# Kernel optimization log

Measured on AMD Instinct MI355X. Metric: run time of the kernel, lower is better.

Reference implementation:

```python
import jax, jax.numpy as jnp
import numpy as np

B, NQ, NK = 4, 2048, 2048
D_MODEL, D_K, D_V, H = 1024, 1024, 1024, 16


def setup_inputs() -> dict:
    key = jax.random.key(0)
    ks = jax.random.split(key, 8)
    return {
        "queries": jax.random.normal(ks[0], (B, NQ, D_MODEL), dtype=jnp.float32),
        "keys": jax.random.normal(ks[1], (B, NK, D_MODEL), dtype=jnp.float32),
        "values": jax.random.normal(ks[2], (B, NK, D_MODEL), dtype=jnp.float32),
        # nn.Linear weights init.normal_(std=0.001); stored here in (in, out) layout
        "Wq": jax.random.normal(ks[3], (D_MODEL, D_K), dtype=jnp.float32) * 0.001,
        "Wk": jax.random.normal(ks[4], (D_MODEL, D_K), dtype=jnp.float32) * 0.001,
        "Wv": jax.random.normal(ks[5], (D_MODEL, D_V), dtype=jnp.float32) * 0.001,
        "Wo": jax.random.normal(ks[6], (D_V, D_MODEL), dtype=jnp.float32) * 0.001,
        "bo": jnp.zeros((D_MODEL,), dtype=jnp.float32),
    }


def reference(queries, keys, values, Wq, Wk, Wv, Wo, bo):
    b_s, nq, _ = queries.shape
    nk = keys.shape[1]
    hd_k = D_K // H  # per-head key dim
    hd_v = D_V // H  # per-head value dim
    # projections -> [b, h, n, hd]
    q = (queries @ Wq).reshape(b_s, nq, H, hd_k).transpose(0, 2, 1, 3)
    k = (keys @ Wk).reshape(b_s, nk, H, hd_k).transpose(0, 2, 1, 3)
    v = (values @ Wv).reshape(b_s, nk, H, hd_v).transpose(0, 2, 1, 3)
    # NOTE: original scales by sqrt(d_k) (full d_k), not per-head dim
    att = jnp.einsum("bhqd,bhkd->bhqk", q, k) / np.float32(np.sqrt(D_K))
    att = jax.nn.softmax(att, axis=-1)
    # dropout = identity (eval mode)
    out = jnp.einsum("bhqk,bhkd->bhqd", att, v)
    out = out.transpose(0, 2, 1, 3).reshape(b_s, nq, D_V)
    return out @ Wo + bo
```

## Files before the change

kernel.cpp:

```cpp
#include <hip/hip_runtime.h>


#define DM    1024
#define NSEQ  2048
#define HEADS 16
#define HD    64

typedef float floatx4 __attribute__((ext_vector_type(4)));
typedef short s16x4   __attribute__((ext_vector_type(4)));
typedef short s16x8   __attribute__((ext_vector_type(8)));
typedef unsigned int u32x4 __attribute__((ext_vector_type(4)));

static __device__ __forceinline__ floatx4 mfma_bf16(s16x8 a, s16x8 b, floatx4 c) {
  return __builtin_amdgcn_mfma_f32_16x16x32_bf16(a, b, c, 0, 0, 0);
}

static __device__ __forceinline__ void gload_lds16(const void* g, void* l) {
  __builtin_amdgcn_global_load_lds(
      (const __attribute__((address_space(1))) unsigned*)g,
      (__attribute__((address_space(3))) unsigned*)l, 16, 0, 0);
}

static __device__ __forceinline__ unsigned lds_addr(const void* p) {
  return (unsigned)(unsigned long long)p;
}

static __device__ __forceinline__ s16x8 ds_read_b128a(unsigned byteaddr) {
  s16x8 r;
  asm volatile("ds_read_b128 %0, %1" : "=v"(r) : "v"(byteaddr));
  return r;
}

#define SCHED0() __builtin_amdgcn_sched_barrier(0)
#define WAIT_LGKM0() \
  { asm volatile("s_waitcnt lgkmcnt(0)" ::: "memory"); __builtin_amdgcn_sched_barrier(0); }
#define WAIT_VMCNT(N) \
  { asm volatile("s_waitcnt vmcnt(" #N ")" ::: "memory"); __builtin_amdgcn_sched_barrier(0); }

static __device__ __forceinline__ short f2bf(float f) {
  unsigned u = __builtin_bit_cast(unsigned, f);
  u += 0x7FFFu + ((u >> 16) & 1u);
  return (short)(u >> 16);
}

static __device__ __forceinline__ unsigned cvtpk_bf16(float lo, float hi) {
  unsigned r;
  asm("v_cvt_pk_bf16_f32 %0, %1, %2" : "=v"(r) : "v"(lo), "v"(hi));
  return r;
}

static __device__ __forceinline__ unsigned pack2_bf16(float a, float b) {
  unsigned ua = __builtin_bit_cast(unsigned, a) + 0x8000u;
  unsigned ub = __builtin_bit_cast(unsigned, b) + 0x8000u;
#if __has_builtin(__builtin_amdgcn_perm)
  return __builtin_amdgcn_perm(ub, ua, 0x07060302u);
#else
  return (ub & 0xffff0000u) | (ua >> 16);
#endif
}

__global__ __launch_bounds__(256) void make_wgroups(
    const float* __restrict__ W0, const float* __restrict__ W1,
    const float* __restrict__ W2, const float* __restrict__ W3,
    short* __restrict__ G0, short* __restrict__ G1,
    short* __restrict__ G2, short* __restrict__ G3) {
  __shared__ float tile[64][68];
  const int m = blockIdx.z;
  const float* W = m == 0 ? W0 : m == 1 ? W1 : m == 2 ? W2 : W3;
  short*       G = m == 0 ? G0 : m == 1 ? G1 : m == 2 ? G2 : G3;
  const int nt = blockIdx.x, kt = blockIdx.y;
  const int n0 = nt * 64, k0 = kt * 64;
  const int t = threadIdx.x;
  for (int j = 0; j < 4; j++) {
    int idx = j * 256 + t, r = idx >> 4, cq = idx & 15;
    *(floatx4*)&tile[r][cq * 4] = *(const floatx4*)(W + (long)(k0 + r) * DM + n0 + cq * 4);
  }
  __syncthreads();
  for (int j = 0; j < 2; j++) {
    int ci = j * 256 + t;
    int lm = ci & 15, quad = (ci >> 4) & 3, kk = (ci >> 6) & 1, gl = ci >> 7;
    s16x8 v;
#pragma unroll
    for (int e = 0; e < 8; e++) v[e] = f2bf(tile[kk * 32 + quad * 8 + e][gl * 16 + lm]);
    long addr;
    if (m < 3) {
      int ct = nt >> 2, g16 = (nt & 3) * 4 + gl;
      addr = ((long)(ct * 16 + kt)) * 16384 + (g16 * 2 + kk) * 512 + (quad * 16 + lm) * 8;
    } else {
      int ct = nt >> 1, g16 = (nt & 1) * 4 + gl;
      addr = ((long)(ct * 16 + kt)) * 8192 + (g16 * 2 + kk) * 512 + (quad * 16 + lm) * 8;
    }
    *(s16x8*)(G + addr) = v;
  }
}

__global__ __launch_bounds__(512, 2) void proj_kernel(
    const float* __restrict__ Aq, const float* __restrict__ Ak, const float* __restrict__ Av,
    const short* __restrict__ BgQ, const short* __restrict__ BgK, const short* __restrict__ BgV,
    short* __restrict__ Qh, short* __restrict__ KVg) {
  __shared__ short lds[2 * 24576];
  const int z = blockIdx.z;
  const float* A  = z == 0 ? Aq  : z == 1 ? Ak  : Av;
  const short* Bg = z == 0 ? BgQ : z == 1 ? BgK : BgV;
  const int t = threadIdx.x;
  const int w = t >> 6, l = t & 63, quad = l >> 4, lm = l & 15;
  const int wm = w >> 2, wn = w & 3;
  const int row0 = blockIdx.x * 128;
  const int ct = blockIdx.y;
  const int col0 = ct * 256;

  floatx4 acc[4][4];
  for (int mi = 0; mi < 4; mi++)
    for (int ni = 0; ni < 4; ni++) acc[mi][ni] = (floatx4){0.f, 0.f, 0.f, 0.f};

  floatx4 ar[2][2];
  auto loadA = [&](int ks) __attribute__((always_inline)) {
#pragma unroll
    for (int j = 0; j < 2; j++) {
      int tt = j * 512 + t, r = tt >> 3, c8 = (tt & 7) * 8;
      const float* p = A + (long)(row0 + r) * DM + ks * 64 + c8;
      ar[j][0] = *(const floatx4*)p;
      ar[j][1] = *(const floatx4*)(p + 4);
    }
  };
  auto writeA = [&](int buf) __attribute__((always_inline)) {
#pragma unroll
    for (int j = 0; j < 2; j++) {
      int tt = j * 512 + t, r = tt >> 3;
      int kk = (tt & 7) >> 2, q4 = tt & 3, lm2 = r & 15, g16 = r >> 4;
      u32x4 pk = {cvtpk_bf16(ar[j][0][0], ar[j][0][1]), cvtpk_bf16(ar[j][0][2], ar[j][0][3]),
                  cvtpk_bf16(ar[j][1][0], ar[j][1][1]), cvtpk_bf16(ar[j][1][2], ar[j][1][3])};
      int l3 = q4 * 16 + (lm2 ^ (q4 * 2));
      *(s16x8*)(lds + buf * 24576 + (g16 * 2 + kk) * 512 + l3 * 8) =
          __builtin_bit_cast(s16x8, pk);
    }
  };
  auto stageB = [&](int ks, int buf) __attribute__((always_inline)) {
    const long pan = ((long)(ct * 16 + ks)) * 16384;
#pragma unroll
    for (int i = 0; i < 4; i++) {
      int gb = w * 4 + i;
      const short* src = Bg + pan + gb * 512 + l * 8;
      gload_lds16(src, lds + buf * 24576 + 8192 + gb * 512);
    }
  };

  const unsigned lds0 = lds_addr(lds);
  auto process = [&](int buf) __attribute__((always_inline)) {
    const unsigned lbase = lds0 + buf * 49152u;
    const unsigned aswz = (quad * 16 + (lm ^ (quad * 2))) * 16;
#pragma unroll
    for (int kk = 0; kk < 2; kk++) {
      s16x8 af[4], bfr[4];
#pragma unroll
      for (int mi = 0; mi < 4; mi++)
        af[mi] = ds_read_b128a(lbase + ((wm * 4 + mi) * 2 + kk) * 1024 + aswz);
#pragma unroll
      for (int ni = 0; ni < 4; ni++)
        bfr[ni] = ds_read_b128a(lbase + 16384 + ((wn * 4 + ni) * 2 + kk) * 1024 + l * 16);
      WAIT_LGKM0();
      __builtin_amdgcn_s_setprio(1);
#pragma unroll
      for (int mi = 0; mi < 4; mi++)
#pragma unroll
        for (int ni = 0; ni < 4; ni++)
          acc[mi][ni] = mfma_bf16(af[mi], bfr[ni], acc[mi][ni]);
      __builtin_amdgcn_s_setprio(0);
    }
  };

  loadA(0);
  stageB(0, 0);
  writeA(0);
  __syncthreads();
  int cur = 0;
  for (int ks = 0; ks < 16; ++ks) {
    if (ks + 1 < 16) { loadA(ks + 1); stageB(ks + 1, cur ^ 1); }
    SCHED0();
    process(cur);
    if (ks + 1 < 16) writeA(cur ^ 1);
    __syncthreads();
    cur ^= 1;
  }

  const int rowbase = row0 + wm * 64;
  const int colbase = col0 + wn * 64;
  const int b = rowbase >> 11;
  const int h = colbase >> 6;
  const int rloc = rowbase & 2047;
  if (z == 0) {
    const float osc = 0.0450842200277801f;
    long base = ((long)(b * HEADS + h)) * NSEQ * HD;
    for (int mi = 0; mi < 4; mi++)
      for (int r = 0; r < 4; r++) {
        int q = rloc + mi * 16 + quad * 4 + r;
        long rowoff = base + (long)q * HD + lm;
        for (int ni = 0; ni < 4; ni++)
          Qh[rowoff + ni * 16] = f2bf(acc[mi][ni][r] * osc);
      }
  } else if (z == 1) {
    long bhb = ((long)(b * HEADS + h)) * 262144;
    for (int mi = 0; mi < 4; mi++)
      for (int r = 0; r < 4; r++) {
        int q = rloc + mi * 16 + quad * 4 + r;
        int tile = q >> 7, s = (q >> 5) & 3, jj = (q >> 4) & 1, lmk = q & 15;
        for (int ni = 0; ni < 4; ni++) {
          int c = ni >> 1, quadk = (ni * 2 + (lm >> 3)) & 3, ek = lm & 7;
          long addr = bhb + (long)tile * 16384 + (s * 4 + jj * 2 + c) * 512 +
                      (quadk * 16 + lmk) * 8 + ek;
          KVg[addr] = f2bf(acc[mi][ni][r]);
        }
      }
  } else {
    long bhb = ((long)(b * HEADS + h)) * 262144;
    for (int mi = 0; mi < 4; mi++)
      for (int r = 0; r < 4; r++) {
        int kc = rloc + (mi >> 1) * 32 + quad * 8 + (mi & 1) * 4 + r;
        int tile = kc >> 7, s = (kc >> 5) & 3, ev = (mi & 1) * 4 + r;
        for (int ni = 0; ni < 4; ni++) {
          long addr = bhb + (long)tile * 16384 + (16 + s * 4 + ni) * 512 +
                      (quad * 16 + lm) * 8 + ev;
          KVg[addr] = f2bf(acc[mi][ni][r]);
        }
      }
  }
}

__global__ __launch_bounds__(512, 2) void attn_kernel(
    const short* __restrict__ Qh, const short* __restrict__ KVg,
    short* __restrict__ Obf) {
  __shared__ short lds[2 * 16384];
  const int t = threadIdx.x;
  const int w = t >> 6, l = t & 63, quad = l >> 4, lm = l & 15;
  const int bh = blockIdx.x;
  const int qtile = blockIdx.y * 256 + w * 32;
  const short* Qp  = Qh  + (long)bh * NSEQ * HD;
  const short* KVp = KVg + (long)bh * 262144;

  s16x8 aq[2][2];
#pragma unroll
  for (int qi = 0; qi < 2; qi++)
#pragma unroll
    for (int c = 0; c < 2; c++)
      aq[qi][c] = *(const s16x8*)(Qp + (long)(qtile + qi * 16 + lm) * HD + c * 32 + quad * 8);

  floatx4 acc[2][4];
  float lsum[2] = {0.f, 0.f};
#pragma unroll
  for (int qi = 0; qi < 2; qi++)
#pragma unroll
    for (int n = 0; n < 4; n++) acc[qi][n] = (floatx4){0.f, 0.f, 0.f, 0.f};

  auto stage = [&](int kt, int buf) __attribute__((always_inline)) {
    short* base = lds + buf * 16384;
    const short* tsrc = KVp + (long)(kt >> 7) * 16384;
#pragma unroll
    for (int i = 0; i < 4; i++) {
      int g = w * 4 + i;
      gload_lds16(tsrc + g * 512 + l * 8, base + g * 512);
    }
  };

  auto process = [&](const short* Lb, int s) __attribute__((always_inline)) {
    s16x8 bk[2][2];
#pragma unroll
    for (int j = 0; j < 2; j++)
#pragma unroll
      for (int c = 0; c < 2; c++)
        bk[j][c] = *(const s16x8*)(Lb + ((s * 4 + j * 2 + c) * 64 + l) * 8);
    s16x8 vraw[4];
#pragma unroll
    for (int n = 0; n < 4; n++)
      vraw[n] = *(const s16x8*)(Lb + ((16 + s * 4 + n) * 64 + l) * 8);
#pragma unroll
    for (int qi = 0; qi < 2; qi++) {
      floatx4 sT[2];
      sT[0] = (floatx4){0.f, 0.f, 0.f, 0.f};
      sT[1] = (floatx4){0.f, 0.f, 0.f, 0.f};
      __builtin_amdgcn_s_setprio(1);
#pragma unroll
      for (int c = 0; c < 2; c++) {
        sT[0] = mfma_bf16(bk[0][c], aq[qi][c], sT[0]);
        sT[1] = mfma_bf16(bk[1][c], aq[qi][c], sT[1]);
      }
      __builtin_amdgcn_s_setprio(0);
      float p0 = __builtin_amdgcn_exp2f(sT[0][0]);
      float p1 = __builtin_amdgcn_exp2f(sT[0][1]);
      float p2 = __builtin_amdgcn_exp2f(sT[0][2]);
      float p3 = __builtin_amdgcn_exp2f(sT[0][3]);
      float p4 = __builtin_amdgcn_exp2f(sT[1][0]);
      float p5 = __builtin_amdgcn_exp2f(sT[1][1]);
      float p6 = __builtin_amdgcn_exp2f(sT[1][2]);
      float p7 = __builtin_amdgcn_exp2f(sT[1][3]);
      lsum[qi] += ((p0 + p1) + (p2 + p3)) + ((p4 + p5) + (p6 + p7));
      u32x4 pw = {pack2_bf16(p0, p1), pack2_bf16(p2, p3),
                  pack2_bf16(p4, p5), pack2_bf16(p6, p7)};
      s16x8 pcat = __builtin_bit_cast(s16x8, pw);
      __builtin_amdgcn_s_setprio(1);
#pragma unroll
      for (int n = 0; n < 4; n++)
        acc[qi][n] = mfma_bf16(vraw[n], pcat, acc[qi][n]);
      __builtin_amdgcn_s_setprio(0);
    }
  };

  stage(0, 0);
  __syncthreads();
  int cur = 0;
  for (int kt = 0; kt < NSEQ; kt += 128) {
    if (kt + 128 < NSEQ) stage(kt + 128, cur ^ 1);
    const short* Lb = lds + cur * 16384;
    process(Lb, 0);
    process(Lb, 1);
    process(Lb, 2);
    process(Lb, 3);
    __syncthreads();
    cur ^= 1;
  }

  const int b = bh >> 4, h = bh & 15;
  short* Ow = lds + w * 1152;
  const int erow = l >> 2, ecg = l & 3;
#pragma unroll
  for (int qi = 0; qi < 2; qi++) {
    float ls = lsum[qi];
    ls += __shfl_xor(ls, 16);
    ls += __shfl_xor(ls, 32);
    float rl = 1.0f / ls;
#pragma unroll
    for (int n = 0; n < 4; n++)
#pragma unroll
      for (int r = 0; r < 4; r++)
        Ow[lm * 72 + n * 16 + quad * 4 + r] = f2bf(acc[qi][n][r] * rl);
    s16x8 o0 = *(const s16x8*)(Ow + erow * 72 + ecg * 16);
    s16x8 o1 = *(const s16x8*)(Ow + erow * 72 + ecg * 16 + 8);
    long gaddr = ((long)(b * NSEQ + qtile + qi * 16 + erow)) * DM + h * HD + ecg * 16;
    *(s16x8*)(Obf + gaddr) = o0;
    *(s16x8*)(Obf + gaddr + 8) = o1;
  }
}

__global__ __launch_bounds__(256, 2) void out_kernel(
    const short* __restrict__ Ab, const short* __restrict__ WoG,
    const float* __restrict__ bias, float* __restrict__ Out) {
  __shared__ short lds[3 * 8192];
  const int t = threadIdx.x;
  const int w = t >> 6, l = t & 63, quad = l >> 4, lm = l & 15;
  const int wm = w >> 1, wn = w & 1;
  const int row0 = blockIdx.x * 128;
  const int ct = blockIdx.y;
  const int col0 = ct * 128;

  floatx4 acc[4][4];
  for (int mi = 0; mi < 4; mi++)
    for (int ni = 0; ni < 4; ni++) acc[mi][ni] = (floatx4){0.f, 0.f, 0.f, 0.f};

  s16x8 ar[2];
  auto loadA = [&](int kt) __attribute__((always_inline)) {
#pragma unroll
    for (int j = 0; j < 2; j++) {
      int tt = j * 256 + t, r = tt >> 2, c = tt & 3;
      ar[j] = *(const s16x8*)(Ab + (long)(row0 + r) * DM + kt * 32 + c * 8);
    }
  };
  auto writeA = [&](int buf) __attribute__((always_inline)) {
#pragma unroll
    for (int j = 0; j < 2; j++) {
      int tt = j * 256 + t, r = tt >> 2, q4 = tt & 3;
      int lm2 = r & 15, g16 = r >> 4;
      int l3 = q4 * 16 + (lm2 ^ (q4 * 2));
      *(s16x8*)(lds + buf * 8192 + g16 * 512 + l3 * 8) = ar[j];
    }
  };
  auto stageB = [&](int kt, int buf) __attribute__((always_inline)) {
    const long pan = ((long)(ct * 16 + (kt >> 1))) * 8192;
    const int kk = kt & 1;
#pragma unroll
    for (int i = 0; i < 2; i++) {
      int gb = w * 2 + i;
      const short* src = WoG + pan + (gb * 2 + kk) * 512 + l * 8;
      gload_lds16(src, lds + buf * 8192 + 4096 + gb * 512);
    }
  };
  const unsigned lds0 = lds_addr(lds);
  auto process = [&](int buf) __attribute__((always_inline)) {
    const unsigned lbase = lds0 + buf * 16384;
    const unsigned aswz = (quad * 16 + (lm ^ (quad * 2))) * 16;
    s16x8 af[4], bfr[4];
#pragma unroll
    for (int mi = 0; mi < 4; mi++)
      af[mi] = ds_read_b128a(lbase + (wm * 4 + mi) * 1024 + aswz);
#pragma unroll
    for (int ni = 0; ni < 4; ni++)
      bfr[ni] = ds_read_b128a(lbase + 8192 + (wn * 4 + ni) * 1024 + l * 16);
    WAIT_LGKM0();
    __builtin_amdgcn_s_setprio(1);
#pragma unroll
    for (int mi = 0; mi < 4; mi++)
#pragma unroll
      for (int ni = 0; ni < 4; ni++)
        acc[mi][ni] = mfma_bf16(af[mi], bfr[ni], acc[mi][ni]);
    __builtin_amdgcn_s_setprio(0);
  };

  loadA(0);
  stageB(0, 0);
  stageB(1, 1);
  writeA(0);
  WAIT_VMCNT(2);
  WAIT_LGKM0();
  __builtin_amdgcn_s_barrier();

  for (int kt = 0; kt < 32; ++kt) {
    if (kt + 1 < 32) loadA(kt + 1);
    if (kt + 2 < 32) stageB(kt + 2, (kt + 2) % 3);
    SCHED0();
    process(kt % 3);
    if (kt + 1 < 32) writeA((kt + 1) % 3);
    WAIT_VMCNT(2);
    WAIT_LGKM0();
    __builtin_amdgcn_s_barrier();
  }

  const int rowbase = row0 + wm * 64;
  const int colbase = col0 + wn * 64;
  for (int mi = 0; mi < 4; mi++)
    for (int r = 0; r < 4; r++) {
      int gr = rowbase + mi * 16 + quad * 4 + r;
      for (int ni = 0; ni < 4; ni++) {
        int gc = colbase + ni * 16 + lm;
        Out[(long)gr * DM + gc] = acc[mi][ni][r] + bias[gc];
      }
    }
}

extern "C" void kernel_launch(void* const* d_in, const int* in_sizes, int n_in,
                              void* d_out, int out_size, void* d_ws, size_t ws_size,
                              hipStream_t stream) {
  (void)in_sizes; (void)n_in; (void)out_size; (void)ws_size;
  const float* queries = (const float*)d_in[0];
  const float* keys    = (const float*)d_in[1];
  const float* values  = (const float*)d_in[2];
  const float* Wq = (const float*)d_in[3];
  const float* Wk = (const float*)d_in[4];
  const float* Wv = (const float*)d_in[5];
  const float* Wo = (const float*)d_in[6];
  const float* bo = (const float*)d_in[7];
  float* out = (float*)d_out;

  char* ws = (char*)d_ws;
  const size_t MB = 1024 * 1024;
  short* WqG = (short*)(ws + 0 * MB);
  short* WkG = (short*)(ws + 2 * MB);
  short* WvG = (short*)(ws + 4 * MB);
  short* WoG = (short*)(ws + 6 * MB);
  short* Qh  = (short*)(ws + 8 * MB);
  short* KVg = (short*)(ws + 24 * MB);
  short* Obf = (short*)(ws + 56 * MB);

  make_wgroups<<<dim3(16, 16, 4), 256, 0, stream>>>(
      Wq, Wk, Wv, Wo, WqG, WkG, WvG, WoG);
  proj_kernel<<<dim3(64, 4, 3), 512, 0, stream>>>(
      queries, keys, values, WqG, WkG, WvG, Qh, KVg);
  attn_kernel<<<dim3(64, 8), 512, 0, stream>>>(Qh, KVg, Obf);
  out_kernel<<<dim3(64, 8), 256, 0, stream>>>(Obf, WoG, bo, out);
}
```

Measured before the change: 318.9 us.

## Read K/V tiles directly from global memory instead of LDS double buffering

Removes the LDS staging of K/V tiles (global_load_lds double buffer plus per-tile barriers) and has each wave load its K and V fragments straight from global memory, relying on the caches. LDS shrinks to a small per-wave output staging buffer and the loop no longer has __syncthreads. In exchange, all 8 waves redundantly fetch the same tile from L2/L1, and load latency is no longer hidden by explicit prefetching.

New measurement: 335.7 us. 5.3% more time.

```diff
diff --git a/kernel.cpp b/kernel.cpp
--- a/kernel.cpp
+++ b/kernel.cpp
@@ -229,7 +229,7 @@
 __global__ __launch_bounds__(512, 2) void attn_kernel(
     const short* __restrict__ Qh, const short* __restrict__ KVg,
     short* __restrict__ Obf) {
-  __shared__ short lds[2 * 16384];
+  __shared__ short Olds[8 * 1152];
   const int t = threadIdx.x;
   const int w = t >> 6, l = t & 63, quad = l >> 4, lm = l & 15;
   const int bh = blockIdx.x;
@@ -251,27 +251,17 @@
 #pragma unroll
     for (int n = 0; n < 4; n++) acc[qi][n] = (floatx4){0.f, 0.f, 0.f, 0.f};
 
-  auto stage = [&](int kt, int buf) __attribute__((always_inline)) {
-    short* base = lds + buf * 16384;
-    const short* tsrc = KVp + (long)(kt >> 7) * 16384;
-#pragma unroll
-    for (int i = 0; i < 4; i++) {
-      int g = w * 4 + i;
-      gload_lds16(tsrc + g * 512 + l * 8, base + g * 512);
-    }
-  };
-
-  auto process = [&](const short* Lb, int s) __attribute__((always_inline)) {
+  auto process = [&](const short* Tb, int s) __attribute__((always_inline)) {
     s16x8 bk[2][2];
 #pragma unroll
     for (int j = 0; j < 2; j++)
 #pragma unroll
       for (int c = 0; c < 2; c++)
-        bk[j][c] = *(const s16x8*)(Lb + ((s * 4 + j * 2 + c) * 64 + l) * 8);
+        bk[j][c] = *(const s16x8*)(Tb + (s * 4 + j * 2 + c) * 512 + l * 8);
     s16x8 vraw[4];
 #pragma unroll
     for (int n = 0; n < 4; n++)
-      vraw[n] = *(const s16x8*)(Lb + ((16 + s * 4 + n) * 64 + l) * 8);
+      vraw[n] = *(const s16x8*)(Tb + (16 + s * 4 + n) * 512 + l * 8);
 #pragma unroll
     for (int qi = 0; qi < 2; qi++) {
       floatx4 sT[2];
@@ -304,22 +294,16 @@
     }
   };
 
-  stage(0, 0);
-  __syncthreads();
-  int cur = 0;
-  for (int kt = 0; kt < NSEQ; kt += 128) {
-    if (kt + 128 < NSEQ) stage(kt + 128, cur ^ 1);
-    const short* Lb = lds + cur * 16384;
-    process(Lb, 0);
-    process(Lb, 1);
-    process(Lb, 2);
-    process(Lb, 3);
-    __syncthreads();
-    cur ^= 1;
+  for (int tile = 0; tile < 16; ++tile) {
+    const short* Tb = KVp + (long)tile * 16384;
+    process(Tb, 0);
+    process(Tb, 1);
+    process(Tb, 2);
+    process(Tb, 3);
   }
 
   const int b = bh >> 4, h = bh & 15;
-  short* Ow = lds + w * 1152;
+  short* Ow = Olds + w * 1152;
   const int erow = l >> 2, ecg = l & 3;
 #pragma unroll
   for (int qi = 0; qi < 2; qi++) {
```
